# Optimization experiments

Hardware: AMD Instinct MI355X
Metric: run time of the kernel (lower is better)

Reference implementation:

```python
import jax, jax.numpy as jnp
import numpy as np

T, K, E, D, F = 16, 8, 64, 2048, 1024  # tokens, top_k, experts, hidden, intermediate


def setup_inputs() -> dict:
    key = jax.random.key(0)
    k1, k2, k3, k4, k5 = jax.random.split(key, 5)
    hidden_states = jax.random.normal(k1, (T, D), dtype=jnp.float32)
    top_k_index = jax.random.randint(k2, (T, K), 0, E, dtype=jnp.int64)
    # routing weights (already summed/normalized per the module's contract)
    top_k_weights = jax.random.uniform(k3, (T, K), dtype=jnp.float32) / K
    # dense dequantized per-expert weights (up: D->F, down: F->D, no bias)
    W_up = jax.random.normal(k4, (E, D, F), dtype=jnp.float32) * 0.02
    W_down = jax.random.normal(k5, (E, F, D), dtype=jnp.float32) * 0.02
    return {
        "hidden_states": hidden_states,
        "top_k_index": top_k_index,
        "top_k_weights": top_k_weights,
        "W_up": W_up,
        "W_down": W_down,
    }


def reference(hidden_states, top_k_index, top_k_weights, W_up, W_down):
    num_experts = W_up.shape[0]
    # route[t, e] = sum_k top_k_weights[t, k] * (top_k_index[t, k] == e)
    route = jnp.sum(
        jax.nn.one_hot(top_k_index, num_experts, dtype=top_k_weights.dtype)
        * top_k_weights[..., None],
        axis=1,
    )  # [T, E]
    # up_proj for every expert on every token (few tokens -> cheap, weight-bound)
    h = jnp.einsum("td,edf->etf", hidden_states, W_up)  # [E, T, F]
    a = jnp.square(jax.nn.relu(h))  # relu^2 activation (NemotronH non-gated MoE)
    # down_proj then weighted combine; experts not routed get zero weight
    out = jnp.einsum("etf,efd,te->td", a, W_down, route)  # [T, D]
    return out.astype(hidden_states.dtype)
```

## Files before the change

kernel.cpp:

```cpp
#include <hip/hip_runtime.h>

#define T_TOK 16
#define K_TOP 8
#define NEXP  64
#define DHID  2048
#define FINT  1024

typedef unsigned int   uint_t;
typedef unsigned short ushort_t;
typedef float f32x4 __attribute__((ext_vector_type(4)));

#define ROUTE_OFF 0u
#define AIDX_OFF  4096u
#define NA_OFF    (AIDX_OFF + 256u)
#define XT_OFF    8192u
#define ABUF_OFF  (XT_OFF + 131072u)
#define OPART_OFF (ABUF_OFF + 2097152u)

__device__ __forceinline__ ushort_t f2bf(float f) {
    uint_t u = __builtin_bit_cast(uint_t, f);
    u += 0x7FFFu + ((u >> 16) & 1u);
    return (ushort_t)(u >> 16);
}
__device__ __forceinline__ uint_t pk2(float lo, float hi) {
    return (uint_t)f2bf(lo) | ((uint_t)f2bf(hi) << 16);
}
__device__ __forceinline__ float bf_lo(uint_t v) { return __builtin_bit_cast(float, v << 16); }
__device__ __forceinline__ float bf_hi(uint_t v) { return __builtin_bit_cast(float, v & 0xFFFF0000u); }

__global__ void k_prep(const float* __restrict__ x, const int* __restrict__ idx,
                       const float* __restrict__ w, float* __restrict__ xT,
                       float* __restrict__ route, int* __restrict__ aidx,
                       int* __restrict__ nA) {
    const int tid = threadIdx.x;
    const int d = blockIdx.x * 64 + (tid & 63);
    const int tq = tid >> 6;
    float4 v;
    v.x = x[(tq * 4 + 0) * DHID + d];
    v.y = x[(tq * 4 + 1) * DHID + d];
    v.z = x[(tq * 4 + 2) * DHID + d];
    v.w = x[(tq * 4 + 3) * DHID + d];
    *reinterpret_cast<float4*>(xT + d * T_TOK + tq * 4) = v;

    if (blockIdx.x != 0) return;
    __shared__ float r[NEXP * T_TOK];
    __shared__ int is64_s;
    if (tid == 0) {
        int allz = 1;
        for (int i = 1; i < 128; i += 2) allz &= (idx[i] == 0);
        is64_s = allz;
    }
    __syncthreads();
    const int is64 = is64_s;
    for (int i = tid; i < NEXP * T_TOK; i += 256) {
        const int e = i >> 4, t = i & 15;
        float s = 0.f;
#pragma unroll
        for (int k = 0; k < K_TOP; ++k) {
            const int flat = t * K_TOP + k;
            const int ev = is64 ? idx[2 * flat] : idx[flat];
            if (ev == e) s += w[flat];
        }
        r[i] = s;
        route[i] = s;
    }
    __syncthreads();
    if (tid == 0) {
        int n = 0;
        for (int e = 0; e < NEXP; ++e) {
            float s = 0.f;
            for (int t = 0; t < T_TOK; ++t) s += r[e * T_TOK + t];
            if (s != 0.f) aidx[n++] = e;
        }
        *nA = n;
    }
}

#define FMA4(t, xs)                              \
    acc0[t] = fmaf((xs), w4.x, acc0[t]);         \
    acc1[t] = fmaf((xs), w4.y, acc1[t]);         \
    acc2[t] = fmaf((xs), w4.z, acc2[t]);         \
    acc3[t] = fmaf((xs), w4.w, acc3[t]);
#define FMA_PAIR(u, t0_)                                        \
    { const float xl = bf_lo(u), xh = bf_hi(u);                 \
      FMA4(t0_, xl) FMA4((t0_) + 1, xh) }
#define STEP(jj, B)                                                         \
    { const uint4 q0 = xqw[(jj) * 2]; const uint4 q1 = xqw[(jj) * 2 + 1];   \
      const f32x4 w4 = (B);                                                 \
      FMA_PAIR(q0.x, 0) FMA_PAIR(q0.y, 2) FMA_PAIR(q0.z, 4) FMA_PAIR(q0.w, 6) \
      FMA_PAIR(q1.x, 8) FMA_PAIR(q1.y, 10) FMA_PAIR(q1.z, 12) FMA_PAIR(q1.w, 14) }
#define LDW(j) __builtin_nontemporal_load(wrow + (size_t)(j) * WSTEP)

#define RW(reg)                                                         \
    { uint_t* p = lds_u + (reg) * 2048 + lane;                          \
      _Pragma("unroll") for (int tp = 0; tp < 8; ++tp) {                \
          p[(0 * 8 + tp) * 64] = pk2(acc0[2 * tp], acc0[2 * tp + 1]);   \
          p[(1 * 8 + tp) * 64] = pk2(acc1[2 * tp], acc1[2 * tp + 1]);   \
          p[(2 * 8 + tp) * 64] = pk2(acc2[2 * tp], acc2[2 * tp + 1]);   \
          p[(3 * 8 + tp) * 64] = pk2(acc3[2 * tp], acc3[2 * tp + 1]); } }
#define RR(reg)                                                         \
    { const uint_t* p = lds_u + (reg) * 2048 + lane;                    \
      _Pragma("unroll") for (int tp = 0; tp < 8; ++tp) {                \
          uint_t u;                                                     \
          u = p[(0 * 8 + tp) * 64]; acc0[2 * tp] += bf_lo(u); acc0[2 * tp + 1] += bf_hi(u); \
          u = p[(1 * 8 + tp) * 64]; acc1[2 * tp] += bf_lo(u); acc1[2 * tp + 1] += bf_hi(u); \
          u = p[(2 * 8 + tp) * 64]; acc2[2 * tp] += bf_lo(u); acc2[2 * tp + 1] += bf_hi(u); \
          u = p[(3 * 8 + tp) * 64]; acc3[2 * tp] += bf_lo(u); acc3[2 * tp + 1] += bf_hi(u); } }

__global__ __launch_bounds__(1024, 4) void k_up(
    const float* __restrict__ xT, const float* __restrict__ Wu,
    const float* __restrict__ route, const int* __restrict__ aidx,
    const int* __restrict__ nAp, ushort_t* __restrict__ a_buf) {
    const int b = blockIdx.x;
    if (b >= 4 * (*nAp)) return;
    const int e = aidx[b >> 2];
    const int fq = b & 3;
    const int tid = threadIdx.x;
    const int wid = tid >> 6, lane = tid & 63;

    __shared__ __align__(16) uint_t lds_u[16384];

    {
        const float4* src = reinterpret_cast<const float4*>(xT);
        uint2* dst = reinterpret_cast<uint2*>(lds_u);
#pragma unroll
        for (int i = 0; i < 8; ++i) {
            const float4 v = src[tid * 8 + i];
            dst[tid * 8 + i] = make_uint2(pk2(v.x, v.y), pk2(v.z, v.w));
        }
    }
    __syncthreads();

    float acc0[16] = {}, acc1[16] = {}, acc2[16] = {}, acc3[16] = {};

    const f32x4* wrow = reinterpret_cast<const f32x4*>(
        Wu + (size_t)e * ((size_t)DHID * FINT) + (size_t)(wid * 128) * FINT
           + fq * 256 + lane * 4);
    const size_t WSTEP = FINT / 4;
    const uint4* xqw = reinterpret_cast<const uint4*>(lds_u) + (size_t)wid * 256;

    f32x4 b0 = LDW(0), b1 = LDW(1), b2 = LDW(2), b3 = LDW(3);
    for (int j = 0; j < 128; j += 4) {
        const bool pf = (j < 124);
        STEP(j + 0, b0) if (pf) b0 = LDW(j + 4);
        STEP(j + 1, b1) if (pf) b1 = LDW(j + 5);
        STEP(j + 2, b2) if (pf) b2 = LDW(j + 6);
        STEP(j + 3, b3) if (pf) b3 = LDW(j + 7);
    }

    __syncthreads();
    if (wid >= 8) RW(wid - 8)
    __syncthreads();
    if (wid < 8) RR(wid)
    __syncthreads();
    if (wid >= 4 && wid < 8) RW(wid - 4)
    __syncthreads();
    if (wid < 4) RR(wid)
    __syncthreads();
    if (wid >= 2 && wid < 4) RW(wid - 2)
    __syncthreads();
    if (wid < 2) RR(wid)
    __syncthreads();
    if (wid == 1) RW(0)
    __syncthreads();
    if (wid == 0) {
        RR(0)
        float rt[16];
#pragma unroll
        for (int t = 0; t < 16; ++t) rt[t] = route[e * T_TOK + t];
#define ACT(A, t) (rt[t] * fmaxf(A[t], 0.f) * fmaxf(A[t], 0.f))
        uint4* ap = reinterpret_cast<uint4*>(
            a_buf + ((size_t)e * FINT + fq * 256 + lane * 4) * T_TOK);
        uint4 o;
#define ST_COL(A, k0)                                                   \
        o.x = pk2(ACT(A, 0), ACT(A, 1));  o.y = pk2(ACT(A, 2), ACT(A, 3));   \
        o.z = pk2(ACT(A, 4), ACT(A, 5));  o.w = pk2(ACT(A, 6), ACT(A, 7));   \
        ap[k0] = o;                                                          \
        o.x = pk2(ACT(A, 8), ACT(A, 9));  o.y = pk2(ACT(A, 10), ACT(A, 11)); \
        o.z = pk2(ACT(A, 12), ACT(A, 13)); o.w = pk2(ACT(A, 14), ACT(A, 15)); \
        ap[k0 + 1] = o;
        ST_COL(acc0, 0) ST_COL(acc1, 2) ST_COL(acc2, 4) ST_COL(acc3, 6)
#undef ST_COL
#undef ACT
    }
}

__global__ __launch_bounds__(1024, 4) void k_down(
    const ushort_t* __restrict__ a_buf, const float* __restrict__ Wd,
    const int* __restrict__ aidx, const int* __restrict__ nAp,
    float* __restrict__ out_part) {
    const int b = blockIdx.x;
    if (b >= 4 * (*nAp)) return;
    const int e = aidx[b >> 2];
    const int dc = b & 3;
    const int tid = threadIdx.x;
    const int wid = tid >> 6, lane = tid & 63;
    const int wd = wid >> 3, wf = wid & 7;

    __shared__ __align__(16) uint_t lds_u[16384];

    {
        const uint4* src = reinterpret_cast<const uint4*>(a_buf + (size_t)e * FINT * T_TOK);
        uint4* dst = reinterpret_cast<uint4*>(lds_u);
        dst[tid] = src[tid];
        dst[tid + 1024] = src[tid + 1024];
    }
    __syncthreads();

    float acc0[16] = {}, acc1[16] = {}, acc2[16] = {}, acc3[16] = {};

    const int d0 = dc * 512 + wd * 256 + lane * 4;
    const f32x4* wrow = reinterpret_cast<const f32x4*>(
        Wd + (size_t)e * ((size_t)FINT * DHID) + (size_t)(wf * 128) * DHID + d0);
    const size_t WSTEP = DHID / 4;
    const uint4* xqw = reinterpret_cast<const uint4*>(lds_u) + (size_t)wf * 256;

    f32x4 b0 = LDW(0), b1 = LDW(1), b2 = LDW(2), b3 = LDW(3);
    for (int j = 0; j < 128; j += 4) {
        const bool pf = (j < 124);
        STEP(j + 0, b0) if (pf) b0 = LDW(j + 4);
        STEP(j + 1, b1) if (pf) b1 = LDW(j + 5);
        STEP(j + 2, b2) if (pf) b2 = LDW(j + 6);
        STEP(j + 3, b3) if (pf) b3 = LDW(j + 7);
    }

    __syncthreads();
    if (wf >= 4) RW(wd * 4 + wf - 4)
    __syncthreads();
    if (wf < 4) RR(wd * 4 + wf)
    __syncthreads();
    if (wf == 2 || wf == 3) RW(wd * 4 + wf - 2)
    __syncthreads();
    if (wf < 2) RR(wd * 4 + wf)
    __syncthreads();
    if (wf == 1) RW(wd * 4)
    __syncthreads();
    if (wf == 0) {
        RR(wd * 4)
        float* op = out_part + (size_t)e * (T_TOK * DHID) + d0;
#pragma unroll
        for (int t = 0; t < 16; ++t)
            *reinterpret_cast<float4*>(op + (size_t)t * DHID) =
                make_float4(acc0[t], acc1[t], acc2[t], acc3[t]);
    }
}

__global__ void k_comb(const float* __restrict__ out_part, const int* __restrict__ aidx,
                       const int* __restrict__ nAp, float* __restrict__ out) {
    const int i = blockIdx.x * 256 + threadIdx.x;
    const int nA = *nAp;
    const size_t off = (size_t)i * 4;
    float4 s = make_float4(0.f, 0.f, 0.f, 0.f);
    for (int a = 0; a < nA; ++a) {
        const float4 v = *reinterpret_cast<const float4*>(
            out_part + (size_t)aidx[a] * (T_TOK * DHID) + off);
        s.x += v.x; s.y += v.y; s.z += v.z; s.w += v.w;
    }
    *reinterpret_cast<float4*>(out + off) = s;
}

extern "C" void kernel_launch(void* const* d_in, const int* in_sizes, int n_in,
                              void* d_out, int out_size, void* d_ws, size_t ws_size,
                              hipStream_t stream) {
    (void)in_sizes; (void)n_in; (void)out_size; (void)ws_size;
    const float* x   = (const float*)d_in[0];
    const int*   idx = (const int*)d_in[1];
    const float* w   = (const float*)d_in[2];
    const float* Wu  = (const float*)d_in[3];
    const float* Wd  = (const float*)d_in[4];
    float* out = (float*)d_out;

    char* ws = (char*)d_ws;
    float*    route    = (float*)(ws + ROUTE_OFF);
    int*      aidx     = (int*)(ws + AIDX_OFF);
    int*      nA       = (int*)(ws + NA_OFF);
    float*    xT       = (float*)(ws + XT_OFF);
    ushort_t* a_buf    = (ushort_t*)(ws + ABUF_OFF);
    float*    out_part = (float*)(ws + OPART_OFF);

    k_prep<<<DHID / 64, 256, 0, stream>>>(x, idx, w, xT, route, aidx, nA);
    k_up<<<4 * NEXP, 1024, 0, stream>>>(xT, Wu, route, aidx, nA, a_buf);
    k_down<<<4 * NEXP, 1024, 0, stream>>>(a_buf, Wd, aidx, nA, out_part);
    k_comb<<<(T_TOK * DHID / 4) / 256, 256, 0, stream>>>(out_part, aidx, nA, out);
}
```

Baseline: 197.0 us.

## Split up and down projections along reduction dim with bf16 partials and activation kernel

Each up-projection block now covers a quarter of the hidden dimension across all F columns, and each down-projection block covers a quarter of F across all D columns. Partial sums are written as bf16 and combined in a new k_act kernel (up side) and an extended k_comb (down side). This shortens the in-block LDS tree reductions and changes how weight rows map to blocks, at the cost of an extra launch, more partial-buffer traffic, and extra bf16 rounding of partial sums.

After: 205.5 us. +4.3%, slower.

```diff
diff --git a/kernel.cpp b/kernel.cpp
--- a/kernel.cpp
+++ b/kernel.cpp
@@ -14,7 +14,9 @@
 #define AIDX_OFF  4096u
 #define NA_OFF    (AIDX_OFF + 256u)
 #define XT_OFF    8192u
-#define ABUF_OFF  (XT_OFF + 131072u)
+#define HPART_OFF 262144u
+#define HPART_STRIDE ((size_t)NEXP * FINT * T_TOK)
+#define ABUF_OFF  (HPART_OFF + 8388608u)
 #define OPART_OFF (ABUF_OFF + 2097152u)
 
 __device__ __forceinline__ ushort_t f2bf(float f) {
@@ -109,24 +111,25 @@
 
 __global__ __launch_bounds__(1024, 4) void k_up(
     const float* __restrict__ xT, const float* __restrict__ Wu,
-    const float* __restrict__ route, const int* __restrict__ aidx,
-    const int* __restrict__ nAp, ushort_t* __restrict__ a_buf) {
+    const int* __restrict__ aidx, const int* __restrict__ nAp,
+    ushort_t* __restrict__ h_part) {
     const int b = blockIdx.x;
     if (b >= 4 * (*nAp)) return;
     const int e = aidx[b >> 2];
-    const int fq = b & 3;
+    const int dr = b & 3;
     const int tid = threadIdx.x;
     const int wid = tid >> 6, lane = tid & 63;
+    const int dsub = wid >> 2, fq = wid & 3;
 
     __shared__ __align__(16) uint_t lds_u[16384];
 
     {
-        const float4* src = reinterpret_cast<const float4*>(xT);
+        const float4* src = reinterpret_cast<const float4*>(xT + (size_t)dr * 512 * T_TOK);
         uint2* dst = reinterpret_cast<uint2*>(lds_u);
 #pragma unroll
-        for (int i = 0; i < 8; ++i) {
-            const float4 v = src[tid * 8 + i];
-            dst[tid * 8 + i] = make_uint2(pk2(v.x, v.y), pk2(v.z, v.w));
+        for (int i = 0; i < 2; ++i) {
+            const float4 v = src[tid * 2 + i];
+            dst[tid * 2 + i] = make_uint2(pk2(v.x, v.y), pk2(v.z, v.w));
         }
     }
     __syncthreads();
@@ -134,10 +137,10 @@
     float acc0[16] = {}, acc1[16] = {}, acc2[16] = {}, acc3[16] = {};
 
     const f32x4* wrow = reinterpret_cast<const f32x4*>(
-        Wu + (size_t)e * ((size_t)DHID * FINT) + (size_t)(wid * 128) * FINT
-           + fq * 256 + lane * 4);
+        Wu + (size_t)e * ((size_t)DHID * FINT)
+           + (size_t)(dr * 512 + dsub * 128) * FINT + fq * 256 + lane * 4);
     const size_t WSTEP = FINT / 4;
-    const uint4* xqw = reinterpret_cast<const uint4*>(lds_u) + (size_t)wid * 256;
+    const uint4* xqw = reinterpret_cast<const uint4*>(lds_u) + (size_t)dsub * 256;
 
     f32x4 b0 = LDW(0), b1 = LDW(1), b2 = LDW(2), b3 = LDW(3);
     for (int j = 0; j < 128; j += 4) {
@@ -149,71 +152,88 @@
     }
 
     __syncthreads();
-    if (wid >= 8) RW(wid - 8)
-    __syncthreads();
-    if (wid < 8) RR(wid)
-    __syncthreads();
-    if (wid >= 4 && wid < 8) RW(wid - 4)
-    __syncthreads();
-    if (wid < 4) RR(wid)
-    __syncthreads();
-    if (wid >= 2 && wid < 4) RW(wid - 2)
-    __syncthreads();
-    if (wid < 2) RR(wid)
-    __syncthreads();
-    if (wid == 1) RW(0)
-    __syncthreads();
-    if (wid == 0) {
-        RR(0)
-        float rt[16];
-#pragma unroll
-        for (int t = 0; t < 16; ++t) rt[t] = route[e * T_TOK + t];
-#define ACT(A, t) (rt[t] * fmaxf(A[t], 0.f) * fmaxf(A[t], 0.f))
-        uint4* ap = reinterpret_cast<uint4*>(
-            a_buf + ((size_t)e * FINT + fq * 256 + lane * 4) * T_TOK);
+    if (dsub >= 2) RW(fq * 2 + dsub - 2)
+    __syncthreads();
+    if (dsub < 2) RR(fq * 2 + dsub)
+    __syncthreads();
+    if (dsub == 1) RW(fq)
+    __syncthreads();
+    if (dsub == 0) {
+        RR(fq)
+        uint4* hp = reinterpret_cast<uint4*>(
+            h_part + ((size_t)(dr * NEXP + e) * FINT + fq * 256 + lane * 4) * T_TOK);
         uint4 o;
-#define ST_COL(A, k0)                                                   \
-        o.x = pk2(ACT(A, 0), ACT(A, 1));  o.y = pk2(ACT(A, 2), ACT(A, 3));   \
-        o.z = pk2(ACT(A, 4), ACT(A, 5));  o.w = pk2(ACT(A, 6), ACT(A, 7));   \
-        ap[k0] = o;                                                          \
-        o.x = pk2(ACT(A, 8), ACT(A, 9));  o.y = pk2(ACT(A, 10), ACT(A, 11)); \
-        o.z = pk2(ACT(A, 12), ACT(A, 13)); o.w = pk2(ACT(A, 14), ACT(A, 15)); \
-        ap[k0 + 1] = o;
+#define ST_COL(A, k0)                                                        \
+        o.x = pk2(A[0], A[1]);   o.y = pk2(A[2], A[3]);                      \
+        o.z = pk2(A[4], A[5]);   o.w = pk2(A[6], A[7]);                      \
+        hp[k0] = o;                                                          \
+        o.x = pk2(A[8], A[9]);   o.y = pk2(A[10], A[11]);                    \
+        o.z = pk2(A[12], A[13]); o.w = pk2(A[14], A[15]);                    \
+        hp[k0 + 1] = o;
         ST_COL(acc0, 0) ST_COL(acc1, 2) ST_COL(acc2, 4) ST_COL(acc3, 6)
 #undef ST_COL
-#undef ACT
-    }
+    }
+}
+
+__global__ void k_act(const ushort_t* __restrict__ h_part, const float* __restrict__ route,
+                      ushort_t* __restrict__ a_buf) {
+    const int e = blockIdx.y;
+    const int i = blockIdx.x * 256 + threadIdx.x;
+    const size_t base = (size_t)e * (FINT * T_TOK) + (size_t)i * 8;
+
+    float s[8] = {};
+#pragma unroll
+    for (int dr = 0; dr < 4; ++dr) {
+        const uint4 hv = *reinterpret_cast<const uint4*>(h_part + dr * HPART_STRIDE + base);
+        s[0] += bf_lo(hv.x); s[1] += bf_hi(hv.x);
+        s[2] += bf_lo(hv.y); s[3] += bf_hi(hv.y);
+        s[4] += bf_lo(hv.z); s[5] += bf_hi(hv.z);
+        s[6] += bf_lo(hv.w); s[7] += bf_hi(hv.w);
+    }
+    const int t0 = (i & 1) * 8;
+    const float* r = route + e * T_TOK + t0;
+    uint4 o;
+    float h0, h1;
+    h0 = fmaxf(s[0], 0.f); h1 = fmaxf(s[1], 0.f);
+    o.x = pk2(r[0] * h0 * h0, r[1] * h1 * h1);
+    h0 = fmaxf(s[2], 0.f); h1 = fmaxf(s[3], 0.f);
+    o.y = pk2(r[2] * h0 * h0, r[3] * h1 * h1);
+    h0 = fmaxf(s[4], 0.f); h1 = fmaxf(s[5], 0.f);
+    o.z = pk2(r[4] * h0 * h0, r[5] * h1 * h1);
+    h0 = fmaxf(s[6], 0.f); h1 = fmaxf(s[7], 0.f);
+    o.w = pk2(r[6] * h0 * h0, r[7] * h1 * h1);
+    *reinterpret_cast<uint4*>(a_buf + base) = o;
 }
 
 __global__ __launch_bounds__(1024, 4) void k_down(
     const ushort_t* __restrict__ a_buf, const float* __restrict__ Wd,
     const int* __restrict__ aidx, const int* __restrict__ nAp,
-    float* __restrict__ out_part) {
+    ushort_t* __restrict__ out_part) {
     const int b = blockIdx.x;
     if (b >= 4 * (*nAp)) return;
     const int e = aidx[b >> 2];
-    const int dc = b & 3;
+    const int fr = b & 3;
     const int tid = threadIdx.x;
     const int wid = tid >> 6, lane = tid & 63;
-    const int wd = wid >> 3, wf = wid & 7;
+    const int fs = wid >> 3, dq = wid & 7;
 
     __shared__ __align__(16) uint_t lds_u[16384];
 
     {
-        const uint4* src = reinterpret_cast<const uint4*>(a_buf + (size_t)e * FINT * T_TOK);
-        uint4* dst = reinterpret_cast<uint4*>(lds_u);
-        dst[tid] = src[tid];
-        dst[tid + 1024] = src[tid + 1024];
+        const uint4* src = reinterpret_cast<const uint4*>(
+            a_buf + ((size_t)e * FINT + fr * 256) * T_TOK);
+        reinterpret_cast<uint4*>(lds_u)[tid] = src[tid];
     }
     __syncthreads();
 
     float acc0[16] = {}, acc1[16] = {}, acc2[16] = {}, acc3[16] = {};
 
-    const int d0 = dc * 512 + wd * 256 + lane * 4;
+    const int d0 = dq * 256 + lane * 4;
     const f32x4* wrow = reinterpret_cast<const f32x4*>(
-        Wd + (size_t)e * ((size_t)FINT * DHID) + (size_t)(wf * 128) * DHID + d0);
+        Wd + (size_t)e * ((size_t)FINT * DHID)
+           + (size_t)(fr * 256 + fs * 128) * DHID + d0);
     const size_t WSTEP = DHID / 4;
-    const uint4* xqw = reinterpret_cast<const uint4*>(lds_u) + (size_t)wf * 256;
+    const uint4* xqw = reinterpret_cast<const uint4*>(lds_u) + (size_t)fs * 256;
 
     f32x4 b0 = LDW(0), b1 = LDW(1), b2 = LDW(2), b3 = LDW(3);
     for (int j = 0; j < 128; j += 4) {
@@ -225,38 +245,40 @@
     }
 
     __syncthreads();
-    if (wf >= 4) RW(wd * 4 + wf - 4)
-    __syncthreads();
-    if (wf < 4) RR(wd * 4 + wf)
-    __syncthreads();
-    if (wf == 2 || wf == 3) RW(wd * 4 + wf - 2)
-    __syncthreads();
-    if (wf < 2) RR(wd * 4 + wf)
-    __syncthreads();
-    if (wf == 1) RW(wd * 4)
-    __syncthreads();
-    if (wf == 0) {
-        RR(wd * 4)
-        float* op = out_part + (size_t)e * (T_TOK * DHID) + d0;
-#pragma unroll
-        for (int t = 0; t < 16; ++t)
-            *reinterpret_cast<float4*>(op + (size_t)t * DHID) =
-                make_float4(acc0[t], acc1[t], acc2[t], acc3[t]);
-    }
-}
-
-__global__ void k_comb(const float* __restrict__ out_part, const int* __restrict__ aidx,
+    if (fs == 1) RW(dq)
+    __syncthreads();
+    if (fs == 0) {
+        RR(dq)
+        ushort_t* op = out_part + ((size_t)(e * 4 + fr) * T_TOK) * DHID + d0;
+#pragma unroll
+        for (int t = 0; t < 16; ++t) {
+            uint2 u;
+            u.x = pk2(acc0[t], acc1[t]);
+            u.y = pk2(acc2[t], acc3[t]);
+            *reinterpret_cast<uint2*>(op + (size_t)t * DHID) = u;
+        }
+    }
+}
+
+__global__ void k_comb(const ushort_t* __restrict__ out_part, const int* __restrict__ aidx,
                        const int* __restrict__ nAp, float* __restrict__ out) {
     const int i = blockIdx.x * 256 + threadIdx.x;
     const int nA = *nAp;
-    const size_t off = (size_t)i * 4;
-    float4 s = make_float4(0.f, 0.f, 0.f, 0.f);
+    const int t = i >> 9;
+    const int d = (i & 511) * 4;
+    const size_t off = (size_t)t * DHID + d;
+    float s0 = 0.f, s1 = 0.f, s2 = 0.f, s3 = 0.f;
     for (int a = 0; a < nA; ++a) {
-        const float4 v = *reinterpret_cast<const float4*>(
-            out_part + (size_t)aidx[a] * (T_TOK * DHID) + off);
-        s.x += v.x; s.y += v.y; s.z += v.z; s.w += v.w;
-    }
-    *reinterpret_cast<float4*>(out + off) = s;
+        const int e = aidx[a];
+#pragma unroll
+        for (int fr = 0; fr < 4; ++fr) {
+            const uint2 v = *reinterpret_cast<const uint2*>(
+                out_part + (size_t)(e * 4 + fr) * (T_TOK * DHID) + off);
+            s0 += bf_lo(v.x); s1 += bf_hi(v.x);
+            s2 += bf_lo(v.y); s3 += bf_hi(v.y);
+        }
+    }
+    *reinterpret_cast<float4*>(out + off) = make_float4(s0, s1, s2, s3);
 }
 
 extern "C" void kernel_launch(void* const* d_in, const int* in_sizes, int n_in,
@@ -275,11 +297,13 @@
     int*      aidx     = (int*)(ws + AIDX_OFF);
     int*      nA       = (int*)(ws + NA_OFF);
     float*    xT       = (float*)(ws + XT_OFF);
+    ushort_t* h_part   = (ushort_t*)(ws + HPART_OFF);
     ushort_t* a_buf    = (ushort_t*)(ws + ABUF_OFF);
-    float*    out_part = (float*)(ws + OPART_OFF);
+    ushort_t* out_part = (ushort_t*)(ws + OPART_OFF);
 
     k_prep<<<DHID / 64, 256, 0, stream>>>(x, idx, w, xT, route, aidx, nA);
-    k_up<<<4 * NEXP, 1024, 0, stream>>>(xT, Wu, route, aidx, nA, a_buf);
+    k_up<<<4 * NEXP, 1024, 0, stream>>>(xT, Wu, aidx, nA, h_part);
+    k_act<<<dim3(8, NEXP), 256, 0, stream>>>(h_part, route, a_buf);
     k_down<<<4 * NEXP, 1024, 0, stream>>>(a_buf, Wd, aidx, nA, out_part);
     k_comb<<<(T_TOK * DHID / 4) / 256, 256, 0, stream>>>(out_part, aidx, nA, out);
 }
```

## Fuse up and down projections into one persistent work-queue kernel with flag sync

Applied to the files above, without the earlier changes.

Merges k_up and k_down into a single persistent kernel of 256 blocks. Blocks pull work items from an atomic counter, so down-projection items can start as soon as their expert's up-projection pieces finish, tracked by per-expert completion counters. Up items are split over two halves of the hidden dimension, and the partial sums are combined through a global pairing buffer. The bf16 transpose of x moves into k_prep, and the per-expert output partials are stored as bf16 to reduce combine traffic. This removes one launch boundary and the idle tail between stages, at the cost of spin-waits, extra atomics and lower precision in the partial outputs.

New measurement: 381.5 us. 1.94x slower.

```diff
diff --git a/kernel.cpp b/kernel.cpp
--- a/kernel.cpp
+++ b/kernel.cpp
@@ -10,12 +10,16 @@
 typedef unsigned short ushort_t;
 typedef float f32x4 __attribute__((ext_vector_type(4)));
 
-#define ROUTE_OFF 0u
-#define AIDX_OFF  4096u
-#define NA_OFF    (AIDX_OFF + 256u)
-#define XT_OFF    8192u
-#define ABUF_OFF  (XT_OFF + 131072u)
-#define OPART_OFF (ABUF_OFF + 2097152u)
+#define ROUTE_OFF  0u
+#define AIDX_OFF   4096u
+#define NA_OFF     4352u
+#define WCTR_OFF   4356u
+#define UPDONE_OFF 4608u
+#define PAIRC_OFF  4864u
+#define XTBF_OFF   8192u
+#define HPAIR_OFF  131072u
+#define ABUF_OFF   4194304u
+#define OPART_OFF  8388608u
 
 __device__ __forceinline__ ushort_t f2bf(float f) {
     uint_t u = __builtin_bit_cast(uint_t, f);
@@ -27,11 +31,13 @@
 }
 __device__ __forceinline__ float bf_lo(uint_t v) { return __builtin_bit_cast(float, v << 16); }
 __device__ __forceinline__ float bf_hi(uint_t v) { return __builtin_bit_cast(float, v & 0xFFFF0000u); }
+__device__ __forceinline__ float bfround(float f) { return __builtin_bit_cast(float, (uint_t)f2bf(f) << 16); }
 
 __global__ void k_prep(const float* __restrict__ x, const int* __restrict__ idx,
-                       const float* __restrict__ w, float* __restrict__ xT,
+                       const float* __restrict__ w, uint_t* __restrict__ xt_bf,
                        float* __restrict__ route, int* __restrict__ aidx,
-                       int* __restrict__ nA) {
+                       int* __restrict__ nA, int* __restrict__ wctr,
+                       int* __restrict__ up_done, int* __restrict__ pairc) {
     const int tid = threadIdx.x;
     const int d = blockIdx.x * 64 + (tid & 63);
     const int tq = tid >> 6;
@@ -40,9 +46,14 @@
     v.y = x[(tq * 4 + 1) * DHID + d];
     v.z = x[(tq * 4 + 2) * DHID + d];
     v.w = x[(tq * 4 + 3) * DHID + d];
-    *reinterpret_cast<float4*>(xT + d * T_TOK + tq * 4) = v;
+    *reinterpret_cast<uint2*>(xt_bf + d * 8 + tq * 2) =
+        make_uint2(pk2(v.x, v.y), pk2(v.z, v.w));
 
     if (blockIdx.x != 0) return;
+    pairc[tid] = 0;
+    if (tid < 64) up_done[tid] = 0;
+    if (tid == 0) *wctr = 0;
+
     __shared__ float r[NEXP * T_TOK];
     __shared__ int is64_s;
     if (tid == 0) {
@@ -90,173 +101,199 @@
       FMA_PAIR(q0.x, 0) FMA_PAIR(q0.y, 2) FMA_PAIR(q0.z, 4) FMA_PAIR(q0.w, 6) \
       FMA_PAIR(q1.x, 8) FMA_PAIR(q1.y, 10) FMA_PAIR(q1.z, 12) FMA_PAIR(q1.w, 14) }
 #define LDW(j) __builtin_nontemporal_load(wrow + (size_t)(j) * WSTEP)
-
-#define RW(reg)                                                         \
-    { uint_t* p = lds_u + (reg) * 2048 + lane;                          \
-      _Pragma("unroll") for (int tp = 0; tp < 8; ++tp) {                \
-          p[(0 * 8 + tp) * 64] = pk2(acc0[2 * tp], acc0[2 * tp + 1]);   \
-          p[(1 * 8 + tp) * 64] = pk2(acc1[2 * tp], acc1[2 * tp + 1]);   \
-          p[(2 * 8 + tp) * 64] = pk2(acc2[2 * tp], acc2[2 * tp + 1]);   \
-          p[(3 * 8 + tp) * 64] = pk2(acc3[2 * tp], acc3[2 * tp + 1]); } }
-#define RR(reg)                                                         \
-    { const uint_t* p = lds_u + (reg) * 2048 + lane;                    \
-      _Pragma("unroll") for (int tp = 0; tp < 8; ++tp) {                \
+#define STREAM64()                                                 \
+    { f32x4 b0 = LDW(0), b1 = LDW(1), b2 = LDW(2), b3 = LDW(3);    \
+      for (int j = 0; j < 64; j += 4) {                            \
+          const bool pf = (j < 60);                                \
+          STEP(j + 0, b0) if (pf) b0 = LDW(j + 4);                 \
+          STEP(j + 1, b1) if (pf) b1 = LDW(j + 5);                 \
+          STEP(j + 2, b2) if (pf) b2 = LDW(j + 6);                 \
+          STEP(j + 3, b3) if (pf) b3 = LDW(j + 7); } }
+
+#define RW_BODY(p)                                                      \
+    { _Pragma("unroll") for (int tp = 0; tp < 8; ++tp) {                \
+          (p)[(0 * 8 + tp) * 64] = pk2(acc0[2 * tp], acc0[2 * tp + 1]); \
+          (p)[(1 * 8 + tp) * 64] = pk2(acc1[2 * tp], acc1[2 * tp + 1]); \
+          (p)[(2 * 8 + tp) * 64] = pk2(acc2[2 * tp], acc2[2 * tp + 1]); \
+          (p)[(3 * 8 + tp) * 64] = pk2(acc3[2 * tp], acc3[2 * tp + 1]); } }
+#define RR_BODY(p)                                                      \
+    { _Pragma("unroll") for (int tp = 0; tp < 8; ++tp) {                \
           uint_t u;                                                     \
-          u = p[(0 * 8 + tp) * 64]; acc0[2 * tp] += bf_lo(u); acc0[2 * tp + 1] += bf_hi(u); \
-          u = p[(1 * 8 + tp) * 64]; acc1[2 * tp] += bf_lo(u); acc1[2 * tp + 1] += bf_hi(u); \
-          u = p[(2 * 8 + tp) * 64]; acc2[2 * tp] += bf_lo(u); acc2[2 * tp + 1] += bf_hi(u); \
-          u = p[(3 * 8 + tp) * 64]; acc3[2 * tp] += bf_lo(u); acc3[2 * tp + 1] += bf_hi(u); } }
-
-__global__ __launch_bounds__(1024, 4) void k_up(
-    const float* __restrict__ xT, const float* __restrict__ Wu,
-    const float* __restrict__ route, const int* __restrict__ aidx,
-    const int* __restrict__ nAp, ushort_t* __restrict__ a_buf) {
-    const int b = blockIdx.x;
-    if (b >= 4 * (*nAp)) return;
-    const int e = aidx[b >> 2];
-    const int fq = b & 3;
+          u = (p)[(0 * 8 + tp) * 64]; acc0[2 * tp] += bf_lo(u); acc0[2 * tp + 1] += bf_hi(u); \
+          u = (p)[(1 * 8 + tp) * 64]; acc1[2 * tp] += bf_lo(u); acc1[2 * tp + 1] += bf_hi(u); \
+          u = (p)[(2 * 8 + tp) * 64]; acc2[2 * tp] += bf_lo(u); acc2[2 * tp + 1] += bf_hi(u); \
+          u = (p)[(3 * 8 + tp) * 64]; acc3[2 * tp] += bf_lo(u); acc3[2 * tp + 1] += bf_hi(u); } }
+#define RW(reg) { uint_t* p_ = lds_u + (reg) * 2048 + lane; RW_BODY(p_) }
+#define RR(reg) { const uint_t* p_ = lds_u + (reg) * 2048 + lane; RR_BODY(p_) }
+
+#define TREE16()                                   \
+    __syncthreads();                               \
+    if (wid >= 8) RW(wid - 8)                      \
+    __syncthreads();                               \
+    if (wid < 8) RR(wid)                           \
+    __syncthreads();                               \
+    if (wid >= 4 && wid < 8) RW(wid - 4)           \
+    __syncthreads();                               \
+    if (wid < 4) RR(wid)                           \
+    __syncthreads();                               \
+    if (wid >= 2 && wid < 4) RW(wid - 2)           \
+    __syncthreads();                               \
+    if (wid < 2) RR(wid)                           \
+    __syncthreads();                               \
+    if (wid == 1) RW(0)                            \
+    __syncthreads();
+
+__global__ __launch_bounds__(1024, 4) void k_fused(
+    const uint_t* __restrict__ xt_bf, const float* __restrict__ Wu,
+    const float* __restrict__ Wd, const float* __restrict__ route,
+    const int* __restrict__ aidx, const int* __restrict__ nAp,
+    int* wctr, int* up_done, int* pairc,
+    uint_t* hpair, ushort_t* a_buf, ushort_t* out_part) {
+
     const int tid = threadIdx.x;
     const int wid = tid >> 6, lane = tid & 63;
 
     __shared__ __align__(16) uint_t lds_u[16384];
-
-    {
-        const float4* src = reinterpret_cast<const float4*>(xT);
-        uint2* dst = reinterpret_cast<uint2*>(lds_u);
+    __shared__ int s_item, s_nitems;
+
+    if (tid == 0) s_nitems = 16 * (*nAp);
+    __syncthreads();
+    const int nitems = s_nitems;
+    const int upN = nitems >> 1;
+
+    for (;;) {
+        if (tid == 0)
+            s_item = __hip_atomic_fetch_add(wctr, 1, __ATOMIC_RELAXED, __HIP_MEMORY_SCOPE_AGENT);
+        __syncthreads();
+        const int item = s_item;
+        if (item >= nitems) break;
+
+        if (item < upN) {
+            const int ei = item >> 3;
+            const int fq = (item >> 1) & 3;
+            const int dh = item & 1;
+            const int e = aidx[ei];
+            {
+                const uint4* src = reinterpret_cast<const uint4*>(xt_bf) + (size_t)dh * 2048;
+                uint4* dst = reinterpret_cast<uint4*>(lds_u);
+                dst[tid] = src[tid];
+                dst[tid + 1024] = src[tid + 1024];
+            }
+            __syncthreads();
+            float acc0[16] = {}, acc1[16] = {}, acc2[16] = {}, acc3[16] = {};
+            const f32x4* wrow = reinterpret_cast<const f32x4*>(
+                Wu + (size_t)e * ((size_t)DHID * FINT)
+                   + (size_t)(dh * 1024 + wid * 64) * FINT + fq * 256 + lane * 4);
+            const size_t WSTEP = FINT / 4;
+            const uint4* xqw = reinterpret_cast<const uint4*>(lds_u) + (size_t)wid * 128;
+            STREAM64()
+            TREE16()
+            if (wid == 0) {
+                RR(0)
+                const int slot = ei * 4 + fq;
+                uint_t* hp = hpair + (size_t)slot * 2048;
+                int r = 0;
+                if (lane == 0)
+                    r = __hip_atomic_fetch_add(pairc + slot, 1, __ATOMIC_ACQ_REL,
+                                               __HIP_MEMORY_SCOPE_AGENT);
+                r = __shfl(r, 0);
+                if (r == 0) {
+                    { uint_t* p_ = hp + lane; RW_BODY(p_) }
+                    __threadfence();
+                    if (lane == 0)
+                        __hip_atomic_fetch_add(pairc + slot, 1, __ATOMIC_RELEASE,
+                                               __HIP_MEMORY_SCOPE_AGENT);
+                } else {
+                    while (__hip_atomic_load(pairc + slot, __ATOMIC_ACQUIRE,
+                                             __HIP_MEMORY_SCOPE_AGENT) < 3)
+                        __builtin_amdgcn_s_sleep(1);
 #pragma unroll
-        for (int i = 0; i < 8; ++i) {
-            const float4 v = src[tid * 8 + i];
-            dst[tid * 8 + i] = make_uint2(pk2(v.x, v.y), pk2(v.z, v.w));
-        }
-    }
-    __syncthreads();
-
-    float acc0[16] = {}, acc1[16] = {}, acc2[16] = {}, acc3[16] = {};
-
-    const f32x4* wrow = reinterpret_cast<const f32x4*>(
-        Wu + (size_t)e * ((size_t)DHID * FINT) + (size_t)(wid * 128) * FINT
-           + fq * 256 + lane * 4);
-    const size_t WSTEP = FINT / 4;
-    const uint4* xqw = reinterpret_cast<const uint4*>(lds_u) + (size_t)wid * 256;
-
-    f32x4 b0 = LDW(0), b1 = LDW(1), b2 = LDW(2), b3 = LDW(3);
-    for (int j = 0; j < 128; j += 4) {
-        const bool pf = (j < 124);
-        STEP(j + 0, b0) if (pf) b0 = LDW(j + 4);
-        STEP(j + 1, b1) if (pf) b1 = LDW(j + 5);
-        STEP(j + 2, b2) if (pf) b2 = LDW(j + 6);
-        STEP(j + 3, b3) if (pf) b3 = LDW(j + 7);
-    }
-
-    __syncthreads();
-    if (wid >= 8) RW(wid - 8)
-    __syncthreads();
-    if (wid < 8) RR(wid)
-    __syncthreads();
-    if (wid >= 4 && wid < 8) RW(wid - 4)
-    __syncthreads();
-    if (wid < 4) RR(wid)
-    __syncthreads();
-    if (wid >= 2 && wid < 4) RW(wid - 2)
-    __syncthreads();
-    if (wid < 2) RR(wid)
-    __syncthreads();
-    if (wid == 1) RW(0)
-    __syncthreads();
-    if (wid == 0) {
-        RR(0)
-        float rt[16];
+                    for (int t = 0; t < 16; ++t) {
+                        acc0[t] = bfround(acc0[t]); acc1[t] = bfround(acc1[t]);
+                        acc2[t] = bfround(acc2[t]); acc3[t] = bfround(acc3[t]);
+                    }
+                    { const uint_t* p_ = hp + lane; RR_BODY(p_) }
+                    float rt[16];
 #pragma unroll
-        for (int t = 0; t < 16; ++t) rt[t] = route[e * T_TOK + t];
+                    for (int t = 0; t < 16; ++t) rt[t] = route[e * T_TOK + t];
 #define ACT(A, t) (rt[t] * fmaxf(A[t], 0.f) * fmaxf(A[t], 0.f))
-        uint4* ap = reinterpret_cast<uint4*>(
-            a_buf + ((size_t)e * FINT + fq * 256 + lane * 4) * T_TOK);
-        uint4 o;
-#define ST_COL(A, k0)                                                   \
-        o.x = pk2(ACT(A, 0), ACT(A, 1));  o.y = pk2(ACT(A, 2), ACT(A, 3));   \
-        o.z = pk2(ACT(A, 4), ACT(A, 5));  o.w = pk2(ACT(A, 6), ACT(A, 7));   \
-        ap[k0] = o;                                                          \
-        o.x = pk2(ACT(A, 8), ACT(A, 9));  o.y = pk2(ACT(A, 10), ACT(A, 11)); \
-        o.z = pk2(ACT(A, 12), ACT(A, 13)); o.w = pk2(ACT(A, 14), ACT(A, 15)); \
-        ap[k0 + 1] = o;
-        ST_COL(acc0, 0) ST_COL(acc1, 2) ST_COL(acc2, 4) ST_COL(acc3, 6)
+                    uint4* ap = reinterpret_cast<uint4*>(
+                        a_buf + ((size_t)e * FINT + fq * 256 + lane * 4) * T_TOK);
+                    uint4 o;
+#define ST_COL(A, k0)                                                            \
+                    o.x = pk2(ACT(A, 0), ACT(A, 1));   o.y = pk2(ACT(A, 2), ACT(A, 3));   \
+                    o.z = pk2(ACT(A, 4), ACT(A, 5));   o.w = pk2(ACT(A, 6), ACT(A, 7));   \
+                    ap[k0] = o;                                                           \
+                    o.x = pk2(ACT(A, 8), ACT(A, 9));   o.y = pk2(ACT(A, 10), ACT(A, 11)); \
+                    o.z = pk2(ACT(A, 12), ACT(A, 13)); o.w = pk2(ACT(A, 14), ACT(A, 15)); \
+                    ap[k0 + 1] = o;
+                    ST_COL(acc0, 0) ST_COL(acc1, 2) ST_COL(acc2, 4) ST_COL(acc3, 6)
 #undef ST_COL
 #undef ACT
-    }
-}
-
-__global__ __launch_bounds__(1024, 4) void k_down(
-    const ushort_t* __restrict__ a_buf, const float* __restrict__ Wd,
-    const int* __restrict__ aidx, const int* __restrict__ nAp,
-    float* __restrict__ out_part) {
-    const int b = blockIdx.x;
-    if (b >= 4 * (*nAp)) return;
-    const int e = aidx[b >> 2];
-    const int dc = b & 3;
-    const int tid = threadIdx.x;
-    const int wid = tid >> 6, lane = tid & 63;
-    const int wd = wid >> 3, wf = wid & 7;
-
-    __shared__ __align__(16) uint_t lds_u[16384];
-
-    {
-        const uint4* src = reinterpret_cast<const uint4*>(a_buf + (size_t)e * FINT * T_TOK);
-        uint4* dst = reinterpret_cast<uint4*>(lds_u);
-        dst[tid] = src[tid];
-        dst[tid + 1024] = src[tid + 1024];
-    }
-    __syncthreads();
-
-    float acc0[16] = {}, acc1[16] = {}, acc2[16] = {}, acc3[16] = {};
-
-    const int d0 = dc * 512 + wd * 256 + lane * 4;
-    const f32x4* wrow = reinterpret_cast<const f32x4*>(
-        Wd + (size_t)e * ((size_t)FINT * DHID) + (size_t)(wf * 128) * DHID + d0);
-    const size_t WSTEP = DHID / 4;
-    const uint4* xqw = reinterpret_cast<const uint4*>(lds_u) + (size_t)wf * 256;
-
-    f32x4 b0 = LDW(0), b1 = LDW(1), b2 = LDW(2), b3 = LDW(3);
-    for (int j = 0; j < 128; j += 4) {
-        const bool pf = (j < 124);
-        STEP(j + 0, b0) if (pf) b0 = LDW(j + 4);
-        STEP(j + 1, b1) if (pf) b1 = LDW(j + 5);
-        STEP(j + 2, b2) if (pf) b2 = LDW(j + 6);
-        STEP(j + 3, b3) if (pf) b3 = LDW(j + 7);
-    }
-
-    __syncthreads();
-    if (wf >= 4) RW(wd * 4 + wf - 4)
-    __syncthreads();
-    if (wf < 4) RR(wd * 4 + wf)
-    __syncthreads();
-    if (wf == 2 || wf == 3) RW(wd * 4 + wf - 2)
-    __syncthreads();
-    if (wf < 2) RR(wd * 4 + wf)
-    __syncthreads();
-    if (wf == 1) RW(wd * 4)
-    __syncthreads();
-    if (wf == 0) {
-        RR(wd * 4)
-        float* op = out_part + (size_t)e * (T_TOK * DHID) + d0;
+                    __threadfence();
+                    if (lane == 0)
+                        __hip_atomic_fetch_add(up_done + ei, 1, __ATOMIC_RELEASE,
+                                               __HIP_MEMORY_SCOPE_AGENT);
+                }
+            }
+        } else {
+            const int it2 = item - upN;
+            const int ei = it2 >> 3;
+            const int dc = it2 & 7;
+            const int e = aidx[ei];
+            if (tid == 0) {
+                while (__hip_atomic_load(up_done + ei, __ATOMIC_ACQUIRE,
+                                         __HIP_MEMORY_SCOPE_AGENT) < 4)
+                    __builtin_amdgcn_s_sleep(2);
+            }
+            __syncthreads();
+            {
+                const uint4* src = reinterpret_cast<const uint4*>(
+                    a_buf + (size_t)e * FINT * T_TOK);
+                uint4* dst = reinterpret_cast<uint4*>(lds_u);
+                dst[tid] = src[tid];
+                dst[tid + 1024] = src[tid + 1024];
+            }
+            __syncthreads();
+            float acc0[16] = {}, acc1[16] = {}, acc2[16] = {}, acc3[16] = {};
+            const f32x4* wrow = reinterpret_cast<const f32x4*>(
+                Wd + (size_t)e * ((size_t)FINT * DHID)
+                   + (size_t)(wid * 64) * DHID + dc * 256 + lane * 4);
+            const size_t WSTEP = DHID / 4;
+            const uint4* xqw = reinterpret_cast<const uint4*>(lds_u) + (size_t)wid * 128;
+            STREAM64()
+            TREE16()
+            if (wid == 0) {
+                RR(0)
+                ushort_t* op = out_part + (size_t)e * (T_TOK * DHID) + dc * 256 + lane * 4;
 #pragma unroll
-        for (int t = 0; t < 16; ++t)
-            *reinterpret_cast<float4*>(op + (size_t)t * DHID) =
-                make_float4(acc0[t], acc1[t], acc2[t], acc3[t]);
-    }
-}
-
-__global__ void k_comb(const float* __restrict__ out_part, const int* __restrict__ aidx,
+                for (int t = 0; t < 16; ++t) {
+                    uint2 u;
+                    u.x = pk2(acc0[t], acc1[t]);
+                    u.y = pk2(acc2[t], acc3[t]);
+                    *reinterpret_cast<uint2*>(op + (size_t)t * DHID) = u;
+                }
+            }
+        }
+        __syncthreads();
+    }
+}
+
+__global__ void k_comb(const ushort_t* __restrict__ out_part, const int* __restrict__ aidx,
                        const int* __restrict__ nAp, float* __restrict__ out) {
     const int i = blockIdx.x * 256 + threadIdx.x;
     const int nA = *nAp;
-    const size_t off = (size_t)i * 4;
-    float4 s = make_float4(0.f, 0.f, 0.f, 0.f);
+    const int t = i >> 9;
+    const int d = (i & 511) * 4;
+    const size_t off = (size_t)t * DHID + d;
+    float s0 = 0.f, s1 = 0.f, s2 = 0.f, s3 = 0.f;
     for (int a = 0; a < nA; ++a) {
-        const float4 v = *reinterpret_cast<const float4*>(
+        const uint2 v = *reinterpret_cast<const uint2*>(
             out_part + (size_t)aidx[a] * (T_TOK * DHID) + off);
-        s.x += v.x; s.y += v.y; s.z += v.z; s.w += v.w;
-    }
-    *reinterpret_cast<float4*>(out + off) = s;
+        s0 += bf_lo(v.x); s1 += bf_hi(v.x);
+        s2 += bf_lo(v.y); s3 += bf_hi(v.y);
+    }
+    *reinterpret_cast<float4*>(out + off) = make_float4(s0, s1, s2, s3);
 }
 
 extern "C" void kernel_launch(void* const* d_in, const int* in_sizes, int n_in,
@@ -274,12 +311,17 @@
     float*    route    = (float*)(ws + ROUTE_OFF);
     int*      aidx     = (int*)(ws + AIDX_OFF);
     int*      nA       = (int*)(ws + NA_OFF);
-    float*    xT       = (float*)(ws + XT_OFF);
+    int*      wctr     = (int*)(ws + WCTR_OFF);
+    int*      up_done  = (int*)(ws + UPDONE_OFF);
+    int*      pairc    = (int*)(ws + PAIRC_OFF);
+    uint_t*   xt_bf    = (uint_t*)(ws + XTBF_OFF);
+    uint_t*   hpair    = (uint_t*)(ws + HPAIR_OFF);
     ushort_t* a_buf    = (ushort_t*)(ws + ABUF_OFF);
-    float*    out_part = (float*)(ws + OPART_OFF);
-
-    k_prep<<<DHID / 64, 256, 0, stream>>>(x, idx, w, xT, route, aidx, nA);
-    k_up<<<4 * NEXP, 1024, 0, stream>>>(xT, Wu, route, aidx, nA, a_buf);
-    k_down<<<4 * NEXP, 1024, 0, stream>>>(a_buf, Wd, aidx, nA, out_part);
+    ushort_t* out_part = (ushort_t*)(ws + OPART_OFF);
+
+    k_prep<<<DHID / 64, 256, 0, stream>>>(x, idx, w, xt_bf, route, aidx, nA,
+                                          wctr, up_done, pairc);
+    k_fused<<<256, 1024, 0, stream>>>(xt_bf, Wu, Wd, route, aidx, nA,
+                                      wctr, up_done, pairc, hpair, a_buf, out_part);
     k_comb<<<(T_TOK * DHID / 4) / 256, 256, 0, stream>>>(out_part, aidx, nA, out);
 }
```

## Store down-proj partials as bf16 and split expert combine into two stages

Applied to the files above, without the earlier changes.

The per-expert down-projection outputs are now written as bf16 instead of fp32, halving partial-output traffic. The single combine kernel that looped serially over all active experts is replaced by a two-stage reduction: 8 groups each sum a strided subset of experts into fp32 partials, then a second kernel sums the 8 partials. This adds parallelism to the combine and cuts bytes read, at the cost of an extra launch and bf16 rounding of per-expert outputs before summation.

After: 184.7 us. 6.3% less time.

```diff
diff --git a/kernel.cpp b/kernel.cpp
--- a/kernel.cpp
+++ b/kernel.cpp
@@ -16,6 +16,7 @@
 #define XT_OFF    8192u
 #define ABUF_OFF  (XT_OFF + 131072u)
 #define OPART_OFF (ABUF_OFF + 2097152u)
+#define PART8_OFF (OPART_OFF + 4194304u)
 
 __device__ __forceinline__ ushort_t f2bf(float f) {
     uint_t u = __builtin_bit_cast(uint_t, f);
@@ -188,7 +189,7 @@
 __global__ __launch_bounds__(1024, 4) void k_down(
     const ushort_t* __restrict__ a_buf, const float* __restrict__ Wd,
     const int* __restrict__ aidx, const int* __restrict__ nAp,
-    float* __restrict__ out_part) {
+    ushort_t* __restrict__ out_part) {
     const int b = blockIdx.x;
     if (b >= 4 * (*nAp)) return;
     const int e = aidx[b >> 2];
@@ -237,23 +238,44 @@
     __syncthreads();
     if (wf == 0) {
         RR(wd * 4)
-        float* op = out_part + (size_t)e * (T_TOK * DHID) + d0;
-#pragma unroll
-        for (int t = 0; t < 16; ++t)
-            *reinterpret_cast<float4*>(op + (size_t)t * DHID) =
-                make_float4(acc0[t], acc1[t], acc2[t], acc3[t]);
-    }
-}
-
-__global__ void k_comb(const float* __restrict__ out_part, const int* __restrict__ aidx,
-                       const int* __restrict__ nAp, float* __restrict__ out) {
+        ushort_t* op = out_part + (size_t)e * (T_TOK * DHID) + d0;
+#pragma unroll
+        for (int t = 0; t < 16; ++t) {
+            uint2 u;
+            u.x = pk2(acc0[t], acc1[t]);
+            u.y = pk2(acc2[t], acc3[t]);
+            *reinterpret_cast<uint2*>(op + (size_t)t * DHID) = u;
+        }
+    }
+}
+
+__global__ void k_comb1(const ushort_t* __restrict__ out_part, const int* __restrict__ aidx,
+                        const int* __restrict__ nAp, float* __restrict__ partial) {
+    const int g = blockIdx.y;
     const int i = blockIdx.x * 256 + threadIdx.x;
     const int nA = *nAp;
+    const int t = i >> 9;
+    const int d = (i & 511) * 4;
+    const size_t off = (size_t)t * DHID + d;
+    float s0 = 0.f, s1 = 0.f, s2 = 0.f, s3 = 0.f;
+    for (int a = g; a < nA; a += 8) {
+        const uint2 v = *reinterpret_cast<const uint2*>(
+            out_part + (size_t)aidx[a] * (T_TOK * DHID) + off);
+        s0 += bf_lo(v.x); s1 += bf_hi(v.x);
+        s2 += bf_lo(v.y); s3 += bf_hi(v.y);
+    }
+    *reinterpret_cast<float4*>(partial + (size_t)g * (T_TOK * DHID) + off) =
+        make_float4(s0, s1, s2, s3);
+}
+
+__global__ void k_comb2(const float* __restrict__ partial, float* __restrict__ out) {
+    const int i = blockIdx.x * 256 + threadIdx.x;
     const size_t off = (size_t)i * 4;
     float4 s = make_float4(0.f, 0.f, 0.f, 0.f);
-    for (int a = 0; a < nA; ++a) {
+#pragma unroll
+    for (int g = 0; g < 8; ++g) {
         const float4 v = *reinterpret_cast<const float4*>(
-            out_part + (size_t)aidx[a] * (T_TOK * DHID) + off);
+            partial + (size_t)g * (T_TOK * DHID) + off);
         s.x += v.x; s.y += v.y; s.z += v.z; s.w += v.w;
     }
     *reinterpret_cast<float4*>(out + off) = s;
@@ -276,10 +298,12 @@
     int*      nA       = (int*)(ws + NA_OFF);
     float*    xT       = (float*)(ws + XT_OFF);
     ushort_t* a_buf    = (ushort_t*)(ws + ABUF_OFF);
-    float*    out_part = (float*)(ws + OPART_OFF);
+    ushort_t* out_part = (ushort_t*)(ws + OPART_OFF);
+    float*    partial  = (float*)(ws + PART8_OFF);
 
     k_prep<<<DHID / 64, 256, 0, stream>>>(x, idx, w, xT, route, aidx, nA);
     k_up<<<4 * NEXP, 1024, 0, stream>>>(xT, Wu, route, aidx, nA, a_buf);
     k_down<<<4 * NEXP, 1024, 0, stream>>>(a_buf, Wd, aidx, nA, out_part);
-    k_comb<<<(T_TOK * DHID / 4) / 256, 256, 0, stream>>>(out_part, aidx, nA, out);
-}
+    k_comb1<<<dim3(32, 8), 256, 0, stream>>>(out_part, aidx, nA, partial);
+    k_comb2<<<32, 256, 0, stream>>>(partial, out);
+}
```
